# Performance work log

Measured on AMD Instinct MI355X. Metric: run time of the kernel, lower is better.

The kernel has to match this reference:

```python
import jax, jax.numpy as jnp
import numpy as np

N_NODES = 100000
N_EDGES = 1600000
NUM_GRAPHS = 1000
NODE_IN, EDGE_IN = 32, 16
NODE_EMB, EDGE_EMB, HID, OUT, L = 64, 32, 64, 1, 3
EPS = 1e-5


def _glorot(key, shape):
    fan_in = shape[0]
    return jax.random.normal(key, shape, jnp.float32) / np.sqrt(fan_in)


def setup_inputs() -> dict:
    key = jax.random.key(0)
    ks = jax.random.split(key, 16)
    inp = {
        "x": jax.random.normal(ks[0], (N_NODES, NODE_IN), jnp.float32),
        "edge_attr": jax.random.normal(ks[1], (N_EDGES, EDGE_IN), jnp.float32),
        "edge_index": jax.random.randint(ks[2], (2, N_EDGES), 0, N_NODES, jnp.int64
                                         if jax.config.jax_enable_x64 else jnp.int32),
        "batch": jnp.sort(jax.random.randint(ks[3], (N_NODES,), 0, NUM_GRAPHS)),
        # embeddings
        "node_W": _glorot(ks[4], (NODE_IN, NODE_EMB)),
        "node_b": jnp.zeros((NODE_EMB,), jnp.float32),
        "edge_W": _glorot(ks[5], (EDGE_IN, EDGE_EMB)),
        "edge_b": jnp.zeros((EDGE_EMB,), jnp.float32),
        # per-layer MPNN params (node_dim==64 for every layer since node_emb_dim==hidden_dim)
        "msg_W": _glorot(ks[6], (L, NODE_EMB + EDGE_EMB, HID)),
        "msg_b": jnp.zeros((L, HID), jnp.float32),
        "msg_gamma": jnp.ones((L, HID), jnp.float32),
        "msg_beta": jnp.zeros((L, HID), jnp.float32),
        "upd_W": _glorot(ks[7], (L, NODE_EMB + HID, HID)),
        "upd_b": jnp.zeros((L, HID), jnp.float32),
        "upd_gamma": jnp.ones((L, HID), jnp.float32),
        "upd_beta": jnp.zeros((L, HID), jnp.float32),
        # readout
        "r1_W": _glorot(ks[8], (HID, HID)),
        "r1_b": jnp.zeros((HID,), jnp.float32),
        "r2_W": _glorot(ks[9], (HID, OUT)),
        "r2_b": jnp.zeros((OUT,), jnp.float32),
    }
    return inp


def _bn(h, gamma, beta):
    # BatchNorm1d in training mode: normalize with batch mean / biased variance
    mu = jnp.mean(h, axis=0)
    var = jnp.mean(jnp.square(h - mu), axis=0)
    return gamma * (h - mu) * jax.lax.rsqrt(var + EPS) + beta


def reference(x, edge_attr, edge_index, batch,
              node_W, node_b, edge_W, edge_b,
              msg_W, msg_b, msg_gamma, msg_beta,
              upd_W, upd_b, upd_gamma, upd_beta,
              r1_W, r1_b, r2_W, r2_b):
    h = x @ node_W + node_b                       # [N, 64]
    e = edge_attr @ edge_W + edge_b               # [E, 32]
    src, dst = edge_index[0], edge_index[1]
    for i in range(L):
        # message: gather x_j, concat edge feats, Linear-ReLU-BN (dropout = eval/no-op)
        m = jnp.concatenate([h[src], e], axis=-1) @ msg_W[i] + msg_b[i]   # [E, 64]
        m = _bn(jax.nn.relu(m), msg_gamma[i], msg_beta[i])
        # aggregate: scatter-add to destination nodes
        agg = jax.ops.segment_sum(m, dst, num_segments=N_NODES)          # [N, 64]
        # update: concat self feats, Linear-ReLU-BN
        u = jnp.concatenate([h, agg], axis=-1) @ upd_W[i] + upd_b[i]     # [N, 64]
        h = _bn(jax.nn.relu(u), upd_gamma[i], upd_beta[i])
    # global add pool over graphs
    g = jax.ops.segment_sum(h, batch, num_segments=NUM_GRAPHS)           # [G, 64]
    out = jax.nn.relu(g @ r1_W + r1_b) @ r2_W + r2_b                     # [G, 1]
    return out
```

## Files before the change

### kernel.cpp

```cpp
#include <hip/hip_runtime.h>
#include <hip/hip_bf16.h>

#define N_NODES   100000
#define N_EDGES   1600000
#define NUM_GRAPHS 1000

typedef unsigned int u32;
typedef unsigned short u16;

typedef __bf16 bf16_t;
typedef bf16_t bf16x8 __attribute__((ext_vector_type(8)));
typedef float  f32x4  __attribute__((ext_vector_type(4)));

__device__ __forceinline__ float bf2f(u16 u){ return __uint_as_float(((u32)u)<<16); }
__device__ __forceinline__ float BL(u32 u){ return __uint_as_float(u<<16); }
__device__ __forceinline__ float BH(u32 u){ return __uint_as_float(u&0xffff0000u); }
__device__ __forceinline__ u16 f2bf(float f){
  u32 u = __float_as_uint(f);
  return (u16)((u + 0x7fffu + ((u>>16)&1u)) >> 16);
}
__device__ __forceinline__ float ldf(const void* p, size_t i, int isbf){
  return isbf ? bf2f(((const u16*)p)[i]) : ((const float*)p)[i];
}

union U4BF { uint4 u; bf16x8 v; };

__global__ void k_detect(const u32* __restrict__ x, int* __restrict__ flag){
  int t = threadIdx.x; int cnt = 0;
  for (int i = t; i < 256; i += 64){
    u32 w = x[i];
    u32 e = (w >> 7) & 0xffu;
    if (e >= 110u && e <= 137u) cnt++;
  }
  for (int o = 32; o; o >>= 1) cnt += __shfl_xor(cnt, o);
  if (t == 0) *flag = (cnt > 128) ? 1 : 0;
}

__global__ void k_prep(const void* __restrict__ eW, const void* __restrict__ eb,
                       const void* __restrict__ mW, const void* __restrict__ mb,
                       u16* __restrict__ Weff, const int* __restrict__ flagp){
  int isbf = *flagp;
  int l = blockIdx.x, c = threadIdx.x;
  u16* W = Weff + ((size_t)l*64 + c)*96;
  for (int k = 0; k < 64; k++)
    W[k] = f2bf(ldf(mW, (size_t)(l*96 + k)*64 + c, isbf));
  for (int j = 0; j < 16; j++){
    float acc = 0.f;
    for (int k = 0; k < 32; k++)
      acc += ldf(eW, (size_t)j*32 + k, isbf) * ldf(mW, (size_t)(l*96 + 64 + k)*64 + c, isbf);
    W[64 + j] = f2bf(acc);
  }
  float fbv = ldf(mb, (size_t)l*64 + c, isbf);
  for (int k = 0; k < 32; k++)
    fbv += ldf(eb, k, isbf) * ldf(mW, (size_t)(l*96 + 64 + k)*64 + c, isbf);
  W[80] = f2bf(fbv);
  for (int k = 81; k < 96; k++) W[k] = 0;
}

__global__ void k_updprep(const void* __restrict__ uW, const void* __restrict__ ub,
                          const float* __restrict__ maff,
                          u16* __restrict__ Wupd, float* __restrict__ biasv,
                          float* __restrict__ tvv, const int* __restrict__ flagp, int l){
  int isbf = *flagp; int c = threadIdx.x;
  u16* W = Wupd + (size_t)c*192;
  float tv = 0.f;
  for (int k = 0; k < 64; k++){
    float wka = ldf(uW, (size_t)(l*128 + k)*64 + c, isbf);
    W[k] = f2bf(wka);
    float wkb = ldf(uW, (size_t)(l*128 + 64 + k)*64 + c, isbf);
    float prod = wkb * maff[k];
    u16 hi = f2bf(prod);
    W[64 + k]  = hi;
    W[128 + k] = f2bf(prod - bf2f(hi));
    tv = fmaf(maff[64 + k], wkb, tv);
  }
  biasv[c] = ldf(ub, (size_t)l*64 + c, isbf);
  tvv[c] = tv;
}

__global__ void k_node_emb(const void* __restrict__ x, const void* __restrict__ nW,
                           const void* __restrict__ nb, u16* __restrict__ hsp,
                           const int* __restrict__ flagp){
  int isbf = *flagp;
  int lane = threadIdx.x & 63;
  int gw = (blockIdx.x*blockDim.x + threadIdx.x) >> 6;
  int nw = (gridDim.x*blockDim.x) >> 6;
  float w[32];
#pragma unroll
  for (int k = 0; k < 32; k++) w[k] = ldf(nW, (size_t)k*64 + lane, isbf);
  float bias = ldf(nb, lane, isbf);
  for (int n = gw; n < N_NODES; n += nw){
    float acc = bias;
    if (isbf){
      const uint4* xr = (const uint4*)((const u16*)x + (size_t)n*32);
#pragma unroll
      for (int q = 0; q < 4; q++){
        uint4 a = xr[q];
        u32 uu[4] = {a.x, a.y, a.z, a.w};
#pragma unroll
        for (int j = 0; j < 4; j++){
          acc = fmaf(BL(uu[j]), w[q*8 + 2*j + 0], acc);
          acc = fmaf(BH(uu[j]), w[q*8 + 2*j + 1], acc);
        }
      }
    } else {
      const float4* xr = (const float4*)((const float*)x + (size_t)n*32);
#pragma unroll
      for (int q = 0; q < 8; q++){
        float4 a = xr[q];
        acc = fmaf(a.x, w[q*4+0], acc); acc = fmaf(a.y, w[q*4+1], acc);
        acc = fmaf(a.z, w[q*4+2], acc); acc = fmaf(a.w, w[q*4+3], acc);
      }
    }
    u16 hi = f2bf(acc);
    hsp[(size_t)n*128 + lane]      = hi;
    hsp[(size_t)n*128 + 64 + lane] = f2bf(acc - bf2f(hi));
  }
}

__global__ void k_deg(const int* __restrict__ ei, int* __restrict__ deg){
  int i = blockIdx.x*blockDim.x + threadIdx.x;
  int stride = gridDim.x*blockDim.x;
  for (int e = i; e < N_EDGES; e += stride)
    atomicAdd(&deg[ei[N_EDGES + e]], 1);
}

__global__ void __launch_bounds__(256) k_scan1(const int* __restrict__ deg,
                                               int* __restrict__ bsum){
  __shared__ int wsum[4];
  int b = blockIdx.x, t = threadIdx.x;
  int i0 = b*512 + t;
  int s = 0;
  if (i0 < N_NODES) s += deg[i0];
  if (i0 + 256 < N_NODES) s += deg[i0 + 256];
  for (int o = 32; o; o >>= 1) s += __shfl_xor(s, o);
  if ((t & 63) == 0) wsum[t >> 6] = s;
  __syncthreads();
  if (t == 0) bsum[b] = wsum[0] + wsum[1] + wsum[2] + wsum[3];
}

__global__ void k_scan2(const int* __restrict__ bsum, int* __restrict__ boff,
                        int* __restrict__ rp){
  __shared__ int l[200];
  int t = threadIdx.x;
  if (t < 196) l[t] = bsum[t];
  __syncthreads();
  if (t == 0){
    int r = 0;
    for (int k = 0; k < 196; k++){ int x = l[k]; l[k] = r; r += x; }
    rp[N_NODES] = r;
  }
  __syncthreads();
  if (t < 196) boff[t] = l[t];
}

__global__ void __launch_bounds__(256) k_scan3(const int* __restrict__ deg,
                        const int* __restrict__ boff, int* __restrict__ rp,
                        int* __restrict__ cursor, float* __restrict__ degf){
  __shared__ int wpre[4];
  int b = blockIdx.x, t = threadIdx.x;
  int i0 = b*512 + 2*t;
  int d0 = (i0     < N_NODES) ? deg[i0]     : 0;
  int d1 = (i0 + 1 < N_NODES) ? deg[i0 + 1] : 0;
  int s = d0 + d1;
  int incl = s;
  for (int o = 1; o < 64; o <<= 1){ int u = __shfl_up(incl, o); if ((t & 63) >= o) incl += u; }
  if ((t & 63) == 63) wpre[t >> 6] = incl;
  __syncthreads();
  if (t == 0){ int r = 0; for (int k = 0; k < 4; k++){ int x = wpre[k]; wpre[k] = r; r += x; } }
  __syncthreads();
  int excl = boff[b] + wpre[t >> 6] + incl - s;
  if (i0 < N_NODES){
    rp[i0] = excl; cursor[i0] = excl; degf[i0] = (float)d0;
  }
  if (i0 + 1 < N_NODES){
    rp[i0+1] = excl + d0; cursor[i0+1] = excl + d0; degf[i0+1] = (float)d1;
  }
}

__global__ void k_scatter(const int* __restrict__ ei, int* __restrict__ cursor,
                          int* __restrict__ perm2){
  int i = blockIdx.x*blockDim.x + threadIdx.x;
  int stride = gridDim.x*blockDim.x;
  for (int e = i; e < N_EDGES; e += stride){
    int d = ei[N_EDGES + e];
    int p = atomicAdd(&cursor[d], 1);
    ((int2*)perm2)[p] = make_int2(ei[e], e);
  }
}

__global__ void k_scatter2(const int* __restrict__ ei, int* __restrict__ cursor,
                           int* __restrict__ perm, u16* __restrict__ eacsr,
                           const void* __restrict__ ea, const int* __restrict__ flagp){
  int isbf = *flagp;
  int i = blockIdx.x*blockDim.x + threadIdx.x;
  int stride = gridDim.x*blockDim.x;
  if (i < 16){
    perm[N_EDGES + i] = 0;
    uint4 z = make_uint4(0,0,0,0);
    uint4* out = (uint4*)(eacsr + (size_t)(N_EDGES + i)*16);
    out[0] = z; out[1] = z;
  }
  for (int e = i; e < N_EDGES; e += stride){
    int d = ei[N_EDGES + e];
    int p = atomicAdd(&cursor[d], 1);
    perm[p] = ei[e];
    uint4 r0, r1;
    if (isbf){
      const uint4* er = (const uint4*)((const u16*)ea + (size_t)e*16);
      r0 = er[0]; r1 = er[1];
    } else {
      const float4* ef = (const float4*)((const float*)ea + (size_t)e*16);
      float4 f0 = ef[0], f1 = ef[1], f2 = ef[2], f3 = ef[3];
      r0.x = (u32)f2bf(f0.x) | ((u32)f2bf(f0.y)<<16);
      r0.y = (u32)f2bf(f0.z) | ((u32)f2bf(f0.w)<<16);
      r0.z = (u32)f2bf(f1.x) | ((u32)f2bf(f1.y)<<16);
      r0.w = (u32)f2bf(f1.z) | ((u32)f2bf(f1.w)<<16);
      r1.x = (u32)f2bf(f2.x) | ((u32)f2bf(f2.y)<<16);
      r1.y = (u32)f2bf(f2.z) | ((u32)f2bf(f2.w)<<16);
      r1.z = (u32)f2bf(f3.x) | ((u32)f2bf(f3.y)<<16);
      r1.w = (u32)f2bf(f3.z) | ((u32)f2bf(f3.w)<<16);
    }
    uint4* out = (uint4*)(eacsr + (size_t)p*16);
    out[0] = r0; out[1] = r1;
  }
}

__device__ __forceinline__ void adv_tile(const int* __restrict__ rp,
                                         int ni, int bi, int ei,
                                         int& no, int& bo, int& eo){
  if (bi + 16 < ei){ no = ni; bo = bi + 16; eo = ei; return; }
  int t = ni + 1;
  int nb = ei;
  int ne = rp[(t < N_NODES) ? t + 1 : N_NODES];
  while (nb == ne && t + 1 < N_NODES){
    t++; nb = ne; ne = rp[t + 1];
  }
  no = t; bo = nb; eo = ne;
}

__global__ void __launch_bounds__(256) k_msgmm(
    const u16* __restrict__ hsp, const void* __restrict__ ea,
    const int* __restrict__ rp, const int* __restrict__ perm2,
    const u16* __restrict__ Weff, u16* __restrict__ aggs,
    float* __restrict__ stats, const int* __restrict__ flagp,
    int l, int nwaves){
  __shared__ float bs[128];
  int tid = threadIdx.x;
  if (tid < 128) bs[tid] = 0.f;
  __syncthreads();
  int isbf = *flagp;
  int lane = tid & 63, wv = tid >> 6;
  int w = blockIdx.x*4 + wv;
  long long t0 = (long long)w     * N_EDGES / nwaves;
  long long t1 = (long long)(w+1) * N_EDGES / nwaves;
  int lo = 0, hi = N_NODES;
  while (lo < hi){ int mid = (lo+hi)>>1; if ((long long)rp[mid] < t0) lo = mid+1; else hi = mid; }
  int n0 = lo, n1;
  if (w == nwaves-1) n1 = N_NODES;
  else {
    lo = 0; hi = N_NODES;
    while (lo < hi){ int mid = (lo+hi)>>1; if ((long long)rp[mid] < t1) lo = mid+1; else hi = mid; }
    n1 = lo;
  }
  int nn = lane & 15, kg = lane >> 4;
  bf16x8 B[3][4];
  const u16* Wl = Weff + (size_t)l*64*96;
#pragma unroll
  for (int t = 0; t < 4; t++)
#pragma unroll
    for (int kb = 0; kb < 3; kb++)
      B[kb][t] = *(const bf16x8*)(Wl + (size_t)(t*16+nn)*96 + kb*32 + kg*8);
  U4BF ac; ac.u = make_uint4((kg==2)? 0x3f80u : 0u, 0u, 0u, 0u);
  float s1[4] = {0,0,0,0}, s2[4] = {0,0,0,0};
  for (int n = n0; n < n1; n++){
    int b0 = rp[n], b1 = rp[n+1];
    float r0 = 0.f, r1 = 0.f, r2 = 0.f, r3 = 0.f;
    for (int base = b0; base < b1; base += 16){
      int rem = b1 - base; if (rem > 16) rem = 16;
      int row = (nn < rem) ? nn : rem-1;
      int2 p = ((const int2*)perm2)[base + row];
      const uint4* hp = (const uint4*)(hsp + (size_t)p.x*128);
      U4BF fA, fB, fC;
      fA.u = hp[kg];
      fB.u = hp[4 + kg];
      if (kg < 2){
        if (isbf){
          fC.u = ((const uint4*)ea)[(size_t)p.y*2 + kg];
        } else {
          const float4* ef = (const float4*)ea;
          float4 f0 = ef[(size_t)p.y*4 + kg*2];
          float4 f1 = ef[(size_t)p.y*4 + kg*2 + 1];
          fC.u.x = (u32)f2bf(f0.x) | ((u32)f2bf(f0.y)<<16);
          fC.u.y = (u32)f2bf(f0.z) | ((u32)f2bf(f0.w)<<16);
          fC.u.z = (u32)f2bf(f1.x) | ((u32)f2bf(f1.y)<<16);
          fC.u.w = (u32)f2bf(f1.z) | ((u32)f2bf(f1.w)<<16);
        }
      } else fC = ac;
      f32x4 a0 = {0,0,0,0}, a1 = {0,0,0,0}, a2 = {0,0,0,0}, a3 = {0,0,0,0};
      a0 = __builtin_amdgcn_mfma_f32_16x16x32_bf16(fA.v, B[0][0], a0, 0,0,0);
      a1 = __builtin_amdgcn_mfma_f32_16x16x32_bf16(fA.v, B[0][1], a1, 0,0,0);
      a2 = __builtin_amdgcn_mfma_f32_16x16x32_bf16(fA.v, B[0][2], a2, 0,0,0);
      a3 = __builtin_amdgcn_mfma_f32_16x16x32_bf16(fA.v, B[0][3], a3, 0,0,0);
      a0 = __builtin_amdgcn_mfma_f32_16x16x32_bf16(fB.v, B[1][0], a0, 0,0,0);
      a1 = __builtin_amdgcn_mfma_f32_16x16x32_bf16(fB.v, B[1][1], a1, 0,0,0);
      a2 = __builtin_amdgcn_mfma_f32_16x16x32_bf16(fB.v, B[1][2], a2, 0,0,0);
      a3 = __builtin_amdgcn_mfma_f32_16x16x32_bf16(fB.v, B[1][3], a3, 0,0,0);
      a0 = __builtin_amdgcn_mfma_f32_16x16x32_bf16(fC.v, B[2][0], a0, 0,0,0);
      a1 = __builtin_amdgcn_mfma_f32_16x16x32_bf16(fC.v, B[2][1], a1, 0,0,0);
      a2 = __builtin_amdgcn_mfma_f32_16x16x32_bf16(fC.v, B[2][2], a2, 0,0,0);
      a3 = __builtin_amdgcn_mfma_f32_16x16x32_bf16(fC.v, B[2][3], a3, 0,0,0);
      int rowbase = kg*4;
      float ts0 = 0.f, ts1 = 0.f, ts2 = 0.f, ts3 = 0.f;
#pragma unroll
      for (int j = 0; j < 4; j++){
        bool valid = (rowbase + j) < rem;
        float m0 = fmaxf(a0[j], 0.f); m0 = valid ? m0 : 0.f;
        float m1 = fmaxf(a1[j], 0.f); m1 = valid ? m1 : 0.f;
        float m2 = fmaxf(a2[j], 0.f); m2 = valid ? m2 : 0.f;
        float m3 = fmaxf(a3[j], 0.f); m3 = valid ? m3 : 0.f;
        ts0 += m0; ts1 += m1; ts2 += m2; ts3 += m3;
        s2[0] = fmaf(m0,m0,s2[0]); s2[1] = fmaf(m1,m1,s2[1]);
        s2[2] = fmaf(m2,m2,s2[2]); s2[3] = fmaf(m3,m3,s2[3]);
      }
      s1[0] += ts0; s1[1] += ts1; s1[2] += ts2; s1[3] += ts3;
      ts0 += __shfl_xor(ts0,16); ts0 += __shfl_xor(ts0,32);
      ts1 += __shfl_xor(ts1,16); ts1 += __shfl_xor(ts1,32);
      ts2 += __shfl_xor(ts2,16); ts2 += __shfl_xor(ts2,32);
      ts3 += __shfl_xor(ts3,16); ts3 += __shfl_xor(ts3,32);
      r0 += ts0; r1 += ts1; r2 += ts2; r3 += ts3;
    }
    float v = (kg==0) ? r0 : (kg==1) ? r1 : (kg==2) ? r2 : r3;
    u16 hiv = f2bf(v);
    aggs[(size_t)n*128 + lane]      = hiv;
    aggs[(size_t)n*128 + 64 + lane] = f2bf(v - bf2f(hiv));
  }
#pragma unroll
  for (int t = 0; t < 4; t++){
    atomicAdd(&bs[t*16+nn], s1[t]);
    atomicAdd(&bs[64+t*16+nn], s2[t]);
  }
  __syncthreads();
  if (tid < 128) atomicAdd(&stats[tid], bs[tid]);
}

__global__ void __launch_bounds__(256) k_msgmm2(
    const u16* __restrict__ hsp, const u16* __restrict__ eacsr,
    const int* __restrict__ rp, const int* __restrict__ perm,
    const u16* __restrict__ Weff, u16* __restrict__ aggs,
    float* __restrict__ stats, int l, int nwaves){
  __shared__ float bs[128];
  int tid = threadIdx.x;
  if (tid < 128) bs[tid] = 0.f;
  __syncthreads();
  int lane = tid & 63;
  int w = blockIdx.x*4 + (tid >> 6);
  long long t0 = (long long)w     * N_EDGES / nwaves;
  long long t1 = (long long)(w+1) * N_EDGES / nwaves;
  int lo = 0, hi = N_NODES;
  while (lo < hi){ int mid = (lo+hi)>>1; if ((long long)rp[mid] < t0) lo = mid+1; else hi = mid; }
  int n0 = lo, n1;
  if (w == nwaves-1) n1 = N_NODES;
  else {
    lo = 0; hi = N_NODES;
    while (lo < hi){ int mid = (lo+hi)>>1; if ((long long)rp[mid] < t1) lo = mid+1; else hi = mid; }
    n1 = lo;
  }
  int nn = lane & 15, kg = lane >> 4;
  bf16x8 B[3][4];
  const u16* Wl = Weff + (size_t)l*64*96;
#pragma unroll
  for (int t = 0; t < 4; t++)
#pragma unroll
    for (int kb = 0; kb < 3; kb++)
      B[kb][t] = *(const bf16x8*)(Wl + (size_t)(t*16+nn)*96 + kb*32 + kg*8);
  U4BF ac; ac.u = make_uint4((kg==2)? 0x3f80u : 0u, 0u, 0u, 0u);
  float s1[4] = {0,0,0,0}, s2[4] = {0,0,0,0};

  if (n0 < n1){
    {
      int pv = rp[n0];
      for (int m = n0; m < n1; m++){
        int nx = rp[m+1];
        if (nx == pv){
          aggs[(size_t)m*128 + lane] = 0;
          aggs[(size_t)m*128 + 64 + lane] = 0;
        }
        pv = nx;
      }
    }
    int nA = n0;
    int baseA = rp[nA], b1A = rp[nA+1];
    while (baseA == b1A && nA + 1 < n1){ nA++; baseA = b1A; b1A = rp[nA+1]; }
    if (baseA < b1A){
      int nB, baseB, b1B;
      adv_tile(rp, nA, baseA, b1A, nB, baseB, b1B);
      int pB = perm[baseB + nn];
      U4BF fAA, fAB, fAC;
      {
        int pA = perm[baseA + nn];
        const uint4* hpA = (const uint4*)(hsp + (size_t)pA*128);
        fAA.u = hpA[kg]; fAB.u = hpA[4 + kg];
        if (kg < 2) fAC.u = *(const uint4*)(eacsr + ((size_t)baseA + nn)*16 + (size_t)kg*8);
        else fAC = ac;
      }
      float r0 = 0.f, r1 = 0.f, r2 = 0.f, r3 = 0.f;
      while (true){
        int nC, baseC, b1C;
        adv_tile(rp, nB, baseB, b1B, nC, baseC, b1C);
        int pC = perm[baseC + nn];
        const uint4* hpB = (const uint4*)(hsp + (size_t)pB*128);
        U4BF fBA, fBB, fBC;
        fBA.u = hpB[kg]; fBB.u = hpB[4 + kg];
        if (kg < 2) fBC.u = *(const uint4*)(eacsr + ((size_t)baseB + nn)*16 + (size_t)kg*8);
        else fBC = ac;
        f32x4 a0 = {0,0,0,0}, a1 = {0,0,0,0}, a2 = {0,0,0,0}, a3 = {0,0,0,0};
        a0 = __builtin_amdgcn_mfma_f32_16x16x32_bf16(fAA.v, B[0][0], a0, 0,0,0);
        a1 = __builtin_amdgcn_mfma_f32_16x16x32_bf16(fAA.v, B[0][1], a1, 0,0,0);
        a2 = __builtin_amdgcn_mfma_f32_16x16x32_bf16(fAA.v, B[0][2], a2, 0,0,0);
        a3 = __builtin_amdgcn_mfma_f32_16x16x32_bf16(fAA.v, B[0][3], a3, 0,0,0);
        a0 = __builtin_amdgcn_mfma_f32_16x16x32_bf16(fAB.v, B[1][0], a0, 0,0,0);
        a1 = __builtin_amdgcn_mfma_f32_16x16x32_bf16(fAB.v, B[1][1], a1, 0,0,0);
        a2 = __builtin_amdgcn_mfma_f32_16x16x32_bf16(fAB.v, B[1][2], a2, 0,0,0);
        a3 = __builtin_amdgcn_mfma_f32_16x16x32_bf16(fAB.v, B[1][3], a3, 0,0,0);
        a0 = __builtin_amdgcn_mfma_f32_16x16x32_bf16(fAC.v, B[2][0], a0, 0,0,0);
        a1 = __builtin_amdgcn_mfma_f32_16x16x32_bf16(fAC.v, B[2][1], a1, 0,0,0);
        a2 = __builtin_amdgcn_mfma_f32_16x16x32_bf16(fAC.v, B[2][2], a2, 0,0,0);
        a3 = __builtin_amdgcn_mfma_f32_16x16x32_bf16(fAC.v, B[2][3], a3, 0,0,0);
        int rem = b1A - baseA; if (rem > 16) rem = 16;
        int rowbase = kg*4;
        float ts0 = 0.f, ts1 = 0.f, ts2 = 0.f, ts3 = 0.f;
#pragma unroll
        for (int j = 0; j < 4; j++){
          bool valid = (rowbase + j) < rem;
          float m0 = fmaxf(a0[j], 0.f); m0 = valid ? m0 : 0.f;
          float m1 = fmaxf(a1[j], 0.f); m1 = valid ? m1 : 0.f;
          float m2 = fmaxf(a2[j], 0.f); m2 = valid ? m2 : 0.f;
          float m3 = fmaxf(a3[j], 0.f); m3 = valid ? m3 : 0.f;
          ts0 += m0; ts1 += m1; ts2 += m2; ts3 += m3;
          s2[0] = fmaf(m0,m0,s2[0]); s2[1] = fmaf(m1,m1,s2[1]);
          s2[2] = fmaf(m2,m2,s2[2]); s2[3] = fmaf(m3,m3,s2[3]);
        }
        s1[0] += ts0; s1[1] += ts1; s1[2] += ts2; s1[3] += ts3;
        r0 += ts0; r1 += ts1; r2 += ts2; r3 += ts3;
        if (baseA + 16 >= b1A){
          r0 += __shfl_xor(r0,16); r0 += __shfl_xor(r0,32);
          r1 += __shfl_xor(r1,16); r1 += __shfl_xor(r1,32);
          r2 += __shfl_xor(r2,16); r2 += __shfl_xor(r2,32);
          r3 += __shfl_xor(r3,16); r3 += __shfl_xor(r3,32);
          float v = (kg==0) ? r0 : (kg==1) ? r1 : (kg==2) ? r2 : r3;
          u16 hiv = f2bf(v);
          aggs[(size_t)nA*128 + lane]      = hiv;
          aggs[(size_t)nA*128 + 64 + lane] = f2bf(v - bf2f(hiv));
          r0 = r1 = r2 = r3 = 0.f;
        }
        nA = nB; baseA = baseB; b1A = b1B;
        fAA = fBA; fAB = fBB; fAC = fBC;
        nB = nC; baseB = baseC; b1B = b1C; pB = pC;
        if (nA >= n1) break;
      }
    }
  }
#pragma unroll
  for (int t = 0; t < 4; t++){
    atomicAdd(&bs[t*16+nn], s1[t]);
    atomicAdd(&bs[64+t*16+nn], s2[t]);
  }
  __syncthreads();
  if (tid < 128) atomicAdd(&stats[tid], bs[tid]);
}

__global__ void k_fin(float* __restrict__ stats, const void* __restrict__ gamma,
                      const void* __restrict__ beta, float* __restrict__ aff,
                      float cnt_inv, int goff, const int* __restrict__ flagp){
  int isbf = *flagp; int c = threadIdx.x;
  float mu  = stats[c]      * cnt_inv;
  float var = stats[64 + c] * cnt_inv - mu*mu;
  float rs  = rsqrtf(var + 1e-5f);
  float g = ldf(gamma, (size_t)goff + c, isbf);
  float b = ldf(beta,  (size_t)goff + c, isbf);
  aff[c]      = g*rs;
  aff[64 + c] = b - g*mu*rs;
  stats[c] = 0.f; stats[64 + c] = 0.f;
}

#define UPD_TILES (N_NODES/16)
__global__ void __launch_bounds__(256) k_updmm(
    const u16* __restrict__ hsp, u16* __restrict__ aggs,
    const float* __restrict__ degf, const u16* __restrict__ Wupd,
    const float* __restrict__ biasv, const float* __restrict__ tvv,
    float* __restrict__ stats){
  __shared__ float bs[128];
  int tid = threadIdx.x;
  if (tid < 128) bs[tid] = 0.f;
  __syncthreads();
  int lane = tid & 63;
  int nn = lane & 15, kg = lane >> 4;
  int w = blockIdx.x*4 + (tid >> 6);
  int nwv = gridDim.x*4;
  bf16x8 B[6][4];
#pragma unroll
  for (int t = 0; t < 4; t++)
#pragma unroll
    for (int kb = 0; kb < 6; kb++)
      B[kb][t] = *(const bf16x8*)(Wupd + (size_t)(t*16+nn)*192 + kb*32 + kg*8);
  float bc[4], tc[4];
#pragma unroll
  for (int t = 0; t < 4; t++){ bc[t] = biasv[t*16+nn]; tc[t] = tvv[t*16+nn]; }
  float s1[4] = {0,0,0,0}, s2[4] = {0,0,0,0};
  for (int tile = w; tile < UPD_TILES; tile += nwv){
    int n0 = tile*16;
    int r = n0 + nn;
    const uint4* hp = (const uint4*)hsp;
    const uint4* ap = (const uint4*)aggs;
    U4BF hh0, hh1, hl0, hl1, ah0, ah1, al0, al1;
    hh0.u = hp[(size_t)r*16 + kg];       hh1.u = hp[(size_t)r*16 + 4 + kg];
    hl0.u = hp[(size_t)r*16 + 8 + kg];   hl1.u = hp[(size_t)r*16 + 12 + kg];
    ah0.u = ap[(size_t)r*16 + kg];       ah1.u = ap[(size_t)r*16 + 4 + kg];
    al0.u = ap[(size_t)r*16 + 8 + kg];   al1.u = ap[(size_t)r*16 + 12 + kg];
    float dg[4];
#pragma unroll
    for (int j = 0; j < 4; j++) dg[j] = degf[n0 + kg*4 + j];
    f32x4 a0 = {0,0,0,0}, a1 = {0,0,0,0}, a2 = {0,0,0,0}, a3 = {0,0,0,0};
#define MF(F,KB) \
    a0 = __builtin_amdgcn_mfma_f32_16x16x32_bf16(F.v, B[KB][0], a0, 0,0,0); \
    a1 = __builtin_amdgcn_mfma_f32_16x16x32_bf16(F.v, B[KB][1], a1, 0,0,0); \
    a2 = __builtin_amdgcn_mfma_f32_16x16x32_bf16(F.v, B[KB][2], a2, 0,0,0); \
    a3 = __builtin_amdgcn_mfma_f32_16x16x32_bf16(F.v, B[KB][3], a3, 0,0,0);
    MF(hh0,0) MF(hh1,1) MF(hl0,0) MF(hl1,1)
    MF(ah0,2) MF(ah1,3) MF(ah0,4) MF(ah1,5)
    MF(al0,2) MF(al1,3)
#undef MF
#pragma unroll
    for (int j = 0; j < 4; j++){
      int n = n0 + kg*4 + j;
      float m0 = fmaxf(fmaf(tc[0], dg[j], a0[j] + bc[0]), 0.f);
      float m1 = fmaxf(fmaf(tc[1], dg[j], a1[j] + bc[1]), 0.f);
      float m2 = fmaxf(fmaf(tc[2], dg[j], a2[j] + bc[2]), 0.f);
      float m3 = fmaxf(fmaf(tc[3], dg[j], a3[j] + bc[3]), 0.f);
      s1[0] += m0; s1[1] += m1; s1[2] += m2; s1[3] += m3;
      s2[0] = fmaf(m0,m0,s2[0]); s2[1] = fmaf(m1,m1,s2[1]);
      s2[2] = fmaf(m2,m2,s2[2]); s2[3] = fmaf(m3,m3,s2[3]);
      u16* hw = aggs + (size_t)n*128;
      u16 q0 = f2bf(m0), q1 = f2bf(m1), q2 = f2bf(m2), q3 = f2bf(m3);
      hw[     nn] = q0;  hw[64 +      nn] = f2bf(m0 - bf2f(q0));
      hw[16 + nn] = q1;  hw[64 + 16 + nn] = f2bf(m1 - bf2f(q1));
      hw[32 + nn] = q2;  hw[64 + 32 + nn] = f2bf(m2 - bf2f(q2));
      hw[48 + nn] = q3;  hw[64 + 48 + nn] = f2bf(m3 - bf2f(q3));
    }
  }
#pragma unroll
  for (int t = 0; t < 4; t++){
    atomicAdd(&bs[t*16+nn], s1[t]);
    atomicAdd(&bs[64+t*16+nn], s2[t]);
  }
  __syncthreads();
  if (tid < 128) atomicAdd(&stats[tid], bs[tid]);
}

__global__ void k_norm(const u16* __restrict__ aggs, const float* __restrict__ uaff,
                       u16* __restrict__ hsp){
  int lane = threadIdx.x & 63;
  int gw = (blockIdx.x*blockDim.x + threadIdx.x) >> 6;
  int nw = (gridDim.x*blockDim.x) >> 6;
  float s = uaff[lane], t = uaff[64 + lane];
  for (int n = gw; n < N_NODES; n += nw){
    float v = bf2f(aggs[(size_t)n*128 + lane]) + bf2f(aggs[(size_t)n*128 + 64 + lane]);
    float o = fmaf(s, v, t);
    u16 hi = f2bf(o);
    hsp[(size_t)n*128 + lane]      = hi;
    hsp[(size_t)n*128 + 64 + lane] = f2bf(o - bf2f(hi));
  }
}

__global__ void k_pool(const u16* __restrict__ hsp, const int* __restrict__ batch,
                       float* __restrict__ g){
  int lane = threadIdx.x & 63;
  int gw = (blockIdx.x*blockDim.x + threadIdx.x) >> 6;
  int nw = (gridDim.x*blockDim.x) >> 6;
  int chunk = (N_NODES + nw - 1) / nw;
  int n0 = gw*chunk;
  int n1 = n0 + chunk; if (n1 > N_NODES) n1 = N_NODES;
  int cur = -1; float acc = 0.f;
  for (int n = n0; n < n1; n++){
    int b = batch[n];
    float v = bf2f(hsp[(size_t)n*128 + lane]) + bf2f(hsp[(size_t)n*128 + 64 + lane]);
    if (b != cur){
      if (cur >= 0) atomicAdd(&g[(size_t)cur*64 + lane], acc);
      cur = b; acc = v;
    } else acc += v;
  }
  if (cur >= 0) atomicAdd(&g[(size_t)cur*64 + lane], acc);
}

__global__ void k_read(const float* __restrict__ g, const void* __restrict__ r1W,
                       const void* __restrict__ r1b, const void* __restrict__ r2W,
                       const void* __restrict__ r2b, void* __restrict__ out,
                       const int* __restrict__ flagp){
  int isbf = *flagp;
  int lane = threadIdx.x;
  int gr = blockIdx.x;
  float w[64];
#pragma unroll
  for (int k = 0; k < 64; k++) w[k] = ldf(r1W, (size_t)k*64 + lane, isbf);
  float acc = ldf(r1b, lane, isbf);
  const float4* grow = (const float4*)(g + (size_t)gr*64);
#pragma unroll
  for (int q = 0; q < 16; q++){
    float4 a = grow[q];
    acc = fmaf(a.x, w[4*q+0], acc); acc = fmaf(a.y, w[4*q+1], acc);
    acc = fmaf(a.z, w[4*q+2], acc); acc = fmaf(a.w, w[4*q+3], acc);
  }
  float hid = fmaxf(acc, 0.f);
  float p = hid * ldf(r2W, lane, isbf);
  for (int o = 32; o; o >>= 1) p += __shfl_xor(p, o);
  if (lane == 0){
    float v = p + ldf(r2b, 0, isbf);
    if (isbf) ((__hip_bfloat16*)out)[gr] = __float2bfloat16(v);
    else      ((float*)out)[gr] = v;
  }
}

extern "C" void kernel_launch(void* const* d_in, const int* in_sizes, int n_in,
                              void* d_out, int out_size, void* d_ws, size_t ws_size,
                              hipStream_t stream){
  const void* x    = d_in[0];
  const void* ea   = d_in[1];
  const int*  ei   = (const int*)d_in[2];
  const int*  bt   = (const int*)d_in[3];
  const void* nW   = d_in[4];  const void* nb  = d_in[5];
  const void* eW   = d_in[6];  const void* eb  = d_in[7];
  const void* mW   = d_in[8];  const void* mb  = d_in[9];
  const void* mg   = d_in[10]; const void* mbe = d_in[11];
  const void* uW   = d_in[12]; const void* ub  = d_in[13];
  const void* ug   = d_in[14]; const void* ube = d_in[15];
  const void* r1W  = d_in[16]; const void* r1b = d_in[17];
  const void* r2W  = d_in[18]; const void* r2b = d_in[19];

  const size_t NEED_BIG = 110722212ull;
  const bool big = (ws_size >= NEED_BIG);

  float* ws = (float*)d_ws;
  size_t off = 0;
  auto alloc = [&](size_t n){ float* p = ws + off; off += n; return p; };

  u16*   hsp   = (u16*)alloc(6400000);
  u16*   aggs  = (u16*)alloc(6400000);
  u16*   eacsr = nullptr; int* perm = nullptr; int* perm2 = nullptr;
  if (big){
    eacsr = (u16*)alloc(12800128);
    perm  = (int*)alloc(1600016);
  } else {
    perm2 = (int*)alloc(3200000);
  }
  float* degf   = alloc(100000);
  float* zero0  = ws + off;
  int*   deg_i  = (int*)alloc(100000);
  float* g      = alloc(64000);
  float* mstats = alloc(128);
  float* ustats = alloc(128);
  size_t zeroN  = (size_t)((ws + off) - zero0);
  float* maff   = alloc(128);
  float* uaff   = alloc(128);
  int*   flag   = (int*)alloc(16);
  u16*   Weff   = (u16*)alloc(9216);
  u16*   Wupd   = (u16*)alloc(6144);
  float* biasv  = alloc(64);
  float* tvv    = alloc(64);
  int*   row_ptr= (int*)alloc(100001);
  int*   cursor = (int*)alloc(100000);
  int*   bsum   = (int*)alloc(196);
  int*   boff   = (int*)alloc(196);

  const int MM_BLOCKS = 2048;
  const int MM_WAVES  = MM_BLOCKS * 4;
  const int UPD_BLOCKS = 782;

  k_detect<<<1, 64, 0, stream>>>((const u32*)x, flag);
  hipMemsetAsync(zero0, 0, zeroN*sizeof(float), stream);
  k_prep<<<3, 64, 0, stream>>>(eW, eb, mW, mb, Weff, flag);
  k_node_emb<<<256, 256, 0, stream>>>(x, nW, nb, hsp, flag);
  k_deg<<<512, 256, 0, stream>>>(ei, deg_i);
  k_scan1<<<196, 256, 0, stream>>>(deg_i, bsum);
  k_scan2<<<1, 256, 0, stream>>>(bsum, boff, row_ptr);
  k_scan3<<<196, 256, 0, stream>>>(deg_i, boff, row_ptr, cursor, degf);
  if (big)
    k_scatter2<<<512, 256, 0, stream>>>(ei, cursor, perm, eacsr, ea, flag);
  else
    k_scatter<<<512, 256, 0, stream>>>(ei, cursor, perm2);

  for (int l = 0; l < 3; l++){
    if (big)
      k_msgmm2<<<MM_BLOCKS, 256, 0, stream>>>(hsp, eacsr, row_ptr, perm, Weff,
                                              aggs, mstats, l, MM_WAVES);
    else
      k_msgmm<<<MM_BLOCKS, 256, 0, stream>>>(hsp, ea, row_ptr, perm2, Weff,
                                             aggs, mstats, flag, l, MM_WAVES);
    k_fin<<<1, 64, 0, stream>>>(mstats, mg, mbe, maff, 1.0f/(float)N_EDGES, l*64, flag);
    k_updprep<<<1, 64, 0, stream>>>(uW, ub, maff, Wupd, biasv, tvv, flag, l);
    k_updmm<<<UPD_BLOCKS, 256, 0, stream>>>(hsp, aggs, degf, Wupd, biasv, tvv,
                                            ustats);
    k_fin<<<1, 64, 0, stream>>>(ustats, ug, ube, uaff, 1.0f/(float)N_NODES, l*64, flag);
    k_norm<<<256, 256, 0, stream>>>(aggs, uaff, hsp);
  }

  k_pool<<<128, 256, 0, stream>>>(hsp, bt, g);
  k_read<<<NUM_GRAPHS, 64, 0, stream>>>(g, r1W, r1b, r2W, r2b, d_out, flag);
}
```

Baseline: 1.372 ms.

## Fold update BatchNorm affine into next-layer weights and drop normalize pass

The per-layer k_norm pass, which rewrote node features after the update BatchNorm, is removed. The BN scale and shift are instead folded into the next layer's message and update weights and biases, and into the pooling step, with the raw update output used directly by ping-ponging buffers. Per-wave edge ranges are now precomputed once instead of being binary-searched in every message launch, and streaming loads and stores use nontemporal hints. This adds small weight-folding kernels and some precision risk from storing the unnormalized activations.

```diff
diff --git a/kernel.cpp b/kernel.cpp
--- a/kernel.cpp
+++ b/kernel.cpp
@@ -11,6 +11,7 @@
 typedef __bf16 bf16_t;
 typedef bf16_t bf16x8 __attribute__((ext_vector_type(8)));
 typedef float  f32x4  __attribute__((ext_vector_type(4)));
+typedef u32    u32x4  __attribute__((ext_vector_type(4)));
 
 __device__ __forceinline__ float bf2f(u16 u){ return __uint_as_float(((u32)u)<<16); }
 __device__ __forceinline__ float BL(u32 u){ return __uint_as_float(u<<16); }
@@ -22,6 +23,14 @@
 __device__ __forceinline__ float ldf(const void* p, size_t i, int isbf){
   return isbf ? bf2f(((const u16*)p)[i]) : ((const float*)p)[i];
 }
+__device__ __forceinline__ uint4 ntload4(const void* p){
+  u32x4 v = __builtin_nontemporal_load((const u32x4*)p);
+  return make_uint4(v.x, v.y, v.z, v.w);
+}
+__device__ __forceinline__ void ntstore4(void* p, uint4 v){
+  u32x4 t = {v.x, v.y, v.z, v.w};
+  __builtin_nontemporal_store(t, (u32x4*)p);
+}
 
 union U4BF { uint4 u; bf16x8 v; };
 
@@ -36,9 +45,15 @@
   if (t == 0) *flag = (cnt > 128) ? 1 : 0;
 }
 
+__global__ void k_idaff(float* __restrict__ haff){
+  int c = threadIdx.x;
+  haff[c] = 1.f; haff[64 + c] = 0.f;
+}
+
 __global__ void k_prep(const void* __restrict__ eW, const void* __restrict__ eb,
                        const void* __restrict__ mW, const void* __restrict__ mb,
-                       u16* __restrict__ Weff, const int* __restrict__ flagp){
+                       u16* __restrict__ Weff, float* __restrict__ biasm,
+                       const int* __restrict__ flagp){
   int isbf = *flagp;
   int l = blockIdx.x, c = threadIdx.x;
   u16* W = Weff + ((size_t)l*64 + c)*96;
@@ -54,19 +69,38 @@
   for (int k = 0; k < 32; k++)
     fbv += ldf(eb, k, isbf) * ldf(mW, (size_t)(l*96 + 64 + k)*64 + c, isbf);
   W[80] = f2bf(fbv);
+  biasm[(size_t)l*64 + c] = fbv;
   for (int k = 81; k < 96; k++) W[k] = 0;
 }
 
+__global__ void k_fold(const void* __restrict__ mW, const u16* __restrict__ Wbase,
+                       const float* __restrict__ biasm, const float* __restrict__ haff,
+                       u16* __restrict__ Wf, const int* __restrict__ flagp, int l){
+  int isbf = *flagp; int c = threadIdx.x;
+  const u16* Wb = Wbase + ((size_t)l*64 + c)*96;
+  u16* W = Wf + (size_t)c*96;
+  float bb = biasm[(size_t)l*64 + c];
+  for (int k = 0; k < 64; k++){
+    float w = ldf(mW, (size_t)(l*96 + k)*64 + c, isbf);
+    W[k] = f2bf(haff[k] * w);
+    bb = fmaf(haff[64 + k], w, bb);
+  }
+  for (int k = 64; k < 80; k++) W[k] = Wb[k];
+  W[80] = f2bf(bb);
+  for (int k = 81; k < 96; k++) W[k] = 0;
+}
+
 __global__ void k_updprep(const void* __restrict__ uW, const void* __restrict__ ub,
-                          const float* __restrict__ maff,
+                          const float* __restrict__ maff, const float* __restrict__ haff,
                           u16* __restrict__ Wupd, float* __restrict__ biasv,
                           float* __restrict__ tvv, const int* __restrict__ flagp, int l){
   int isbf = *flagp; int c = threadIdx.x;
   u16* W = Wupd + (size_t)c*192;
-  float tv = 0.f;
+  float tv = 0.f, bb = 0.f;
   for (int k = 0; k < 64; k++){
     float wka = ldf(uW, (size_t)(l*128 + k)*64 + c, isbf);
-    W[k] = f2bf(wka);
+    W[k] = f2bf(haff[k] * wka);
+    bb = fmaf(haff[64 + k], wka, bb);
     float wkb = ldf(uW, (size_t)(l*128 + 64 + k)*64 + c, isbf);
     float prod = wkb * maff[k];
     u16 hi = f2bf(prod);
@@ -74,7 +108,7 @@
     W[128 + k] = f2bf(prod - bf2f(hi));
     tv = fmaf(maff[64 + k], wkb, tv);
   }
-  biasv[c] = ldf(ub, (size_t)l*64 + c, isbf);
+  biasv[c] = ldf(ub, (size_t)l*64 + c, isbf) + bb;
   tvv[c] = tv;
 }
 
@@ -178,6 +212,17 @@
   }
 }
 
+__global__ void k_ranges(const int* __restrict__ rp, int* __restrict__ wr,
+                         int nwaves){
+  int w = blockIdx.x*blockDim.x + threadIdx.x;
+  if (w > nwaves) return;
+  if (w == nwaves){ wr[w] = N_NODES; return; }
+  long long t0 = (long long)w * N_EDGES / nwaves;
+  int lo = 0, hi = N_NODES;
+  while (lo < hi){ int mid = (lo+hi)>>1; if ((long long)rp[mid] < t0) lo = mid+1; else hi = mid; }
+  wr[w] = lo;
+}
+
 __global__ void k_scatter(const int* __restrict__ ei, int* __restrict__ cursor,
                           int* __restrict__ perm2){
   int i = blockIdx.x*blockDim.x + threadIdx.x;
@@ -199,7 +244,7 @@
     perm[N_EDGES + i] = 0;
     uint4 z = make_uint4(0,0,0,0);
     uint4* out = (uint4*)(eacsr + (size_t)(N_EDGES + i)*16);
-    out[0] = z; out[1] = z;
+    ntstore4(out, z); ntstore4(out + 1, z);
   }
   for (int e = i; e < N_EDGES; e += stride){
     int d = ei[N_EDGES + e];
@@ -222,7 +267,7 @@
       r1.w = (u32)f2bf(f3.z) | ((u32)f2bf(f3.w)<<16);
     }
     uint4* out = (uint4*)(eacsr + (size_t)p*16);
-    out[0] = r0; out[1] = r1;
+    ntstore4(out, r0); ntstore4(out + 1, r1);
   }
 }
 
@@ -242,9 +287,9 @@
 __global__ void __launch_bounds__(256) k_msgmm(
     const u16* __restrict__ hsp, const void* __restrict__ ea,
     const int* __restrict__ rp, const int* __restrict__ perm2,
-    const u16* __restrict__ Weff, u16* __restrict__ aggs,
+    const u16* __restrict__ Wl, u16* __restrict__ aggs,
     float* __restrict__ stats, const int* __restrict__ flagp,
-    int l, int nwaves){
+    int nwaves){
   __shared__ float bs[128];
   int tid = threadIdx.x;
   if (tid < 128) bs[tid] = 0.f;
@@ -265,7 +310,6 @@
   }
   int nn = lane & 15, kg = lane >> 4;
   bf16x8 B[3][4];
-  const u16* Wl = Weff + (size_t)l*64*96;
 #pragma unroll
   for (int t = 0; t < 4; t++)
 #pragma unroll
@@ -347,28 +391,17 @@
 __global__ void __launch_bounds__(256) k_msgmm2(
     const u16* __restrict__ hsp, const u16* __restrict__ eacsr,
     const int* __restrict__ rp, const int* __restrict__ perm,
-    const u16* __restrict__ Weff, u16* __restrict__ aggs,
-    float* __restrict__ stats, int l, int nwaves){
+    const u16* __restrict__ Wl, u16* __restrict__ aggs,
+    float* __restrict__ stats, const int* __restrict__ wranges){
   __shared__ float bs[128];
   int tid = threadIdx.x;
   if (tid < 128) bs[tid] = 0.f;
   __syncthreads();
   int lane = tid & 63;
   int w = blockIdx.x*4 + (tid >> 6);
-  long long t0 = (long long)w     * N_EDGES / nwaves;
-  long long t1 = (long long)(w+1) * N_EDGES / nwaves;
-  int lo = 0, hi = N_NODES;
-  while (lo < hi){ int mid = (lo+hi)>>1; if ((long long)rp[mid] < t0) lo = mid+1; else hi = mid; }
-  int n0 = lo, n1;
-  if (w == nwaves-1) n1 = N_NODES;
-  else {
-    lo = 0; hi = N_NODES;
-    while (lo < hi){ int mid = (lo+hi)>>1; if ((long long)rp[mid] < t1) lo = mid+1; else hi = mid; }
-    n1 = lo;
-  }
+  int nBeg = wranges[w], nEnd = wranges[w+1];
   int nn = lane & 15, kg = lane >> 4;
   bf16x8 B[3][4];
-  const u16* Wl = Weff + (size_t)l*64*96;
 #pragma unroll
   for (int t = 0; t < 4; t++)
 #pragma unroll
@@ -377,10 +410,10 @@
   U4BF ac; ac.u = make_uint4((kg==2)? 0x3f80u : 0u, 0u, 0u, 0u);
   float s1[4] = {0,0,0,0}, s2[4] = {0,0,0,0};
 
-  if (n0 < n1){
+  if (nBeg < nEnd){
     {
-      int pv = rp[n0];
-      for (int m = n0; m < n1; m++){
+      int pv = rp[nBeg];
+      for (int m = nBeg; m < nEnd; m++){
         int nx = rp[m+1];
         if (nx == pv){
           aggs[(size_t)m*128 + lane] = 0;
@@ -389,30 +422,30 @@
         pv = nx;
       }
     }
-    int nA = n0;
+    int nA = nBeg;
     int baseA = rp[nA], b1A = rp[nA+1];
-    while (baseA == b1A && nA + 1 < n1){ nA++; baseA = b1A; b1A = rp[nA+1]; }
+    while (baseA == b1A && nA + 1 < nEnd){ nA++; baseA = b1A; b1A = rp[nA+1]; }
     if (baseA < b1A){
       int nB, baseB, b1B;
       adv_tile(rp, nA, baseA, b1A, nB, baseB, b1B);
-      int pB = perm[baseB + nn];
+      int pB = __builtin_nontemporal_load(&perm[baseB + nn]);
       U4BF fAA, fAB, fAC;
       {
-        int pA = perm[baseA + nn];
+        int pA = __builtin_nontemporal_load(&perm[baseA + nn]);
         const uint4* hpA = (const uint4*)(hsp + (size_t)pA*128);
         fAA.u = hpA[kg]; fAB.u = hpA[4 + kg];
-        if (kg < 2) fAC.u = *(const uint4*)(eacsr + ((size_t)baseA + nn)*16 + (size_t)kg*8);
+        if (kg < 2) fAC.u = ntload4(eacsr + ((size_t)baseA + nn)*16 + (size_t)kg*8);
         else fAC = ac;
       }
       float r0 = 0.f, r1 = 0.f, r2 = 0.f, r3 = 0.f;
       while (true){
         int nC, baseC, b1C;
         adv_tile(rp, nB, baseB, b1B, nC, baseC, b1C);
-        int pC = perm[baseC + nn];
+        int pC = __builtin_nontemporal_load(&perm[baseC + nn]);
         const uint4* hpB = (const uint4*)(hsp + (size_t)pB*128);
         U4BF fBA, fBB, fBC;
         fBA.u = hpB[kg]; fBB.u = hpB[4 + kg];
-        if (kg < 2) fBC.u = *(const uint4*)(eacsr + ((size_t)baseB + nn)*16 + (size_t)kg*8);
+        if (kg < 2) fBC.u = ntload4(eacsr + ((size_t)baseB + nn)*16 + (size_t)kg*8);
         else fBC = ac;
         f32x4 a0 = {0,0,0,0}, a1 = {0,0,0,0}, a2 = {0,0,0,0}, a3 = {0,0,0,0};
         a0 = __builtin_amdgcn_mfma_f32_16x16x32_bf16(fAA.v, B[0][0], a0, 0,0,0);
@@ -457,7 +490,7 @@
         nA = nB; baseA = baseB; b1A = b1B;
         fAA = fBA; fAB = fBB; fAC = fBC;
         nB = nC; baseB = baseC; b1B = b1C; pB = pC;
-        if (nA >= n1) break;
+        if (nA >= nEnd) break;
       }
     }
   }
@@ -514,10 +547,10 @@
     const uint4* hp = (const uint4*)hsp;
     const uint4* ap = (const uint4*)aggs;
     U4BF hh0, hh1, hl0, hl1, ah0, ah1, al0, al1;
-    hh0.u = hp[(size_t)r*16 + kg];       hh1.u = hp[(size_t)r*16 + 4 + kg];
-    hl0.u = hp[(size_t)r*16 + 8 + kg];   hl1.u = hp[(size_t)r*16 + 12 + kg];
-    ah0.u = ap[(size_t)r*16 + kg];       ah1.u = ap[(size_t)r*16 + 4 + kg];
-    al0.u = ap[(size_t)r*16 + 8 + kg];   al1.u = ap[(size_t)r*16 + 12 + kg];
+    hh0.u = ntload4(&hp[(size_t)r*16 + kg]);       hh1.u = ntload4(&hp[(size_t)r*16 + 4 + kg]);
+    hl0.u = ntload4(&hp[(size_t)r*16 + 8 + kg]);   hl1.u = ntload4(&hp[(size_t)r*16 + 12 + kg]);
+    ah0.u = ntload4(&ap[(size_t)r*16 + kg]);       ah1.u = ntload4(&ap[(size_t)r*16 + 4 + kg]);
+    al0.u = ntload4(&ap[(size_t)r*16 + 8 + kg]);   al1.u = ntload4(&ap[(size_t)r*16 + 12 + kg]);
     float dg[4];
 #pragma unroll
     for (int j = 0; j < 4; j++) dg[j] = degf[n0 + kg*4 + j];
@@ -558,39 +591,25 @@
   if (tid < 128) atomicAdd(&stats[tid], bs[tid]);
 }
 
-__global__ void k_norm(const u16* __restrict__ aggs, const float* __restrict__ uaff,
-                       u16* __restrict__ hsp){
+__global__ void k_pool(const u16* __restrict__ hsp, const int* __restrict__ batch,
+                       const float* __restrict__ aff, float* __restrict__ g){
   int lane = threadIdx.x & 63;
   int gw = (blockIdx.x*blockDim.x + threadIdx.x) >> 6;
   int nw = (gridDim.x*blockDim.x) >> 6;
-  float s = uaff[lane], t = uaff[64 + lane];
-  for (int n = gw; n < N_NODES; n += nw){
-    float v = bf2f(aggs[(size_t)n*128 + lane]) + bf2f(aggs[(size_t)n*128 + 64 + lane]);
-    float o = fmaf(s, v, t);
-    u16 hi = f2bf(o);
-    hsp[(size_t)n*128 + lane]      = hi;
-    hsp[(size_t)n*128 + 64 + lane] = f2bf(o - bf2f(hi));
-  }
-}
-
-__global__ void k_pool(const u16* __restrict__ hsp, const int* __restrict__ batch,
-                       float* __restrict__ g){
-  int lane = threadIdx.x & 63;
-  int gw = (blockIdx.x*blockDim.x + threadIdx.x) >> 6;
-  int nw = (gridDim.x*blockDim.x) >> 6;
+  float s = aff[lane], t = aff[64 + lane];
   int chunk = (N_NODES + nw - 1) / nw;
   int n0 = gw*chunk;
   int n1 = n0 + chunk; if (n1 > N_NODES) n1 = N_NODES;
-  int cur = -1; float acc = 0.f;
+  int cur = -1; float acc = 0.f, cnt = 0.f;
   for (int n = n0; n < n1; n++){
     int b = batch[n];
     float v = bf2f(hsp[(size_t)n*128 + lane]) + bf2f(hsp[(size_t)n*128 + 64 + lane]);
     if (b != cur){
-      if (cur >= 0) atomicAdd(&g[(size_t)cur*64 + lane], acc);
-      cur = b; acc = v;
-    } else acc += v;
-  }
-  if (cur >= 0) atomicAdd(&g[(size_t)cur*64 + lane], acc);
+      if (cur >= 0) atomicAdd(&g[(size_t)cur*64 + lane], fmaf(s, acc, t*cnt));
+      cur = b; acc = v; cnt = 1.f;
+    } else { acc += v; cnt += 1.f; }
+  }
+  if (cur >= 0) atomicAdd(&g[(size_t)cur*64 + lane], fmaf(s, acc, t*cnt));
 }
 
 __global__ void k_read(const float* __restrict__ g, const void* __restrict__ r1W,
@@ -637,7 +656,7 @@
   const void* r1W  = d_in[16]; const void* r1b = d_in[17];
   const void* r2W  = d_in[18]; const void* r2b = d_in[19];
 
-  const size_t NEED_BIG = 110722212ull;
+  const size_t NEED_BIG = 110768044ull;
   const bool big = (ws_size >= NEED_BIG);
 
   float* ws = (float*)d_ws;
@@ -661,16 +680,19 @@
   float* ustats = alloc(128);
   size_t zeroN  = (size_t)((ws + off) - zero0);
   float* maff   = alloc(128);
-  float* uaff   = alloc(128);
+  float* haff   = alloc(128);
   int*   flag   = (int*)alloc(16);
   u16*   Weff   = (u16*)alloc(9216);
+  u16*   Wfold  = (u16*)alloc(3072);
   u16*   Wupd   = (u16*)alloc(6144);
+  float* biasm  = alloc(192);
   float* biasv  = alloc(64);
   float* tvv    = alloc(64);
   int*   row_ptr= (int*)alloc(100001);
   int*   cursor = (int*)alloc(100000);
   int*   bsum   = (int*)alloc(196);
   int*   boff   = (int*)alloc(196);
+  int*   wrng   = (int*)alloc(8194);
 
   const int MM_BLOCKS = 2048;
   const int MM_WAVES  = MM_BLOCKS * 4;
@@ -678,32 +700,37 @@
 
   k_detect<<<1, 64, 0, stream>>>((const u32*)x, flag);
   hipMemsetAsync(zero0, 0, zeroN*sizeof(float), stream);
-  k_prep<<<3, 64, 0, stream>>>(eW, eb, mW, mb, Weff, flag);
+  k_idaff<<<1, 64, 0, stream>>>(haff);
+  k_prep<<<3, 64, 0, stream>>>(eW, eb, mW, mb, Weff, biasm, flag);
   k_node_emb<<<256, 256, 0, stream>>>(x, nW, nb, hsp, flag);
   k_deg<<<512, 256, 0, stream>>>(ei, deg_i);
   k_scan1<<<196, 256, 0, stream>>>(deg_i, bsum);
   k_scan2<<<1, 256, 0, stream>>>(bsum, boff, row_ptr);
   k_scan3<<<196, 256, 0, stream>>>(deg_i, boff, row_ptr, cursor, degf);
-  if (big)
+  if (big){
+    k_ranges<<<33, 256, 0, stream>>>(row_ptr, wrng, MM_WAVES);
     k_scatter2<<<512, 256, 0, stream>>>(ei, cursor, perm, eacsr, ea, flag);
-  else
+  } else {
     k_scatter<<<512, 256, 0, stream>>>(ei, cursor, perm2);
-
+  }
+
+  u16* H = hsp;
+  u16* G = aggs;
   for (int l = 0; l < 3; l++){
+    k_fold<<<1, 64, 0, stream>>>(mW, Weff, biasm, haff, Wfold, flag, l);
     if (big)
-      k_msgmm2<<<MM_BLOCKS, 256, 0, stream>>>(hsp, eacsr, row_ptr, perm, Weff,
-                                              aggs, mstats, l, MM_WAVES);
+      k_msgmm2<<<MM_BLOCKS, 256, 0, stream>>>(H, eacsr, row_ptr, perm, Wfold,
+                                              G, mstats, wrng);
     else
-      k_msgmm<<<MM_BLOCKS, 256, 0, stream>>>(hsp, ea, row_ptr, perm2, Weff,
-                                             aggs, mstats, flag, l, MM_WAVES);
+      k_msgmm<<<MM_BLOCKS, 256, 0, stream>>>(H, ea, row_ptr, perm2, Wfold,
+                                             G, mstats, flag, MM_WAVES);
     k_fin<<<1, 64, 0, stream>>>(mstats, mg, mbe, maff, 1.0f/(float)N_EDGES, l*64, flag);
-    k_updprep<<<1, 64, 0, stream>>>(uW, ub, maff, Wupd, biasv, tvv, flag, l);
-    k_updmm<<<UPD_BLOCKS, 256, 0, stream>>>(hsp, aggs, degf, Wupd, biasv, tvv,
-                                            ustats);
-    k_fin<<<1, 64, 0, stream>>>(ustats, ug, ube, uaff, 1.0f/(float)N_NODES, l*64, flag);
-    k_norm<<<256, 256, 0, stream>>>(aggs, uaff, hsp);
-  }
-
-  k_pool<<<128, 256, 0, stream>>>(hsp, bt, g);
+    k_updprep<<<1, 64, 0, stream>>>(uW, ub, maff, haff, Wupd, biasv, tvv, flag, l);
+    k_updmm<<<UPD_BLOCKS, 256, 0, stream>>>(H, G, degf, Wupd, biasv, tvv, ustats);
+    k_fin<<<1, 64, 0, stream>>>(ustats, ug, ube, haff, 1.0f/(float)N_NODES, l*64, flag);
+    u16* tmp = H; H = G; G = tmp;
+  }
+
+  k_pool<<<128, 256, 0, stream>>>(H, bt, haff, g);
   k_read<<<NUM_GRAPHS, 64, 0, stream>>>(g, r1W, r1b, r2W, r2b, d_out, flag);
 }
```

Result: slower. 1.413 ms (+3.0%).
